# Performance work log

Measured on AMD Instinct MI355X. Metric: run time of the kernel, lower is better.

Reference implementation:

```python
import jax, jax.numpy as jnp
import numpy as np

IN_SIZE = 256
HIDDEN = 512
T = 32768


def setup_inputs() -> dict:
    key = jax.random.key(0)
    ks = jax.random.split(key, 6)
    lim_ih = 1.0 / np.sqrt(HIDDEN)
    inp = {
        "input": jax.random.normal(ks[0], (T, IN_SIZE), dtype=jnp.float32),
        "init_hidden": jax.random.normal(ks[1], (HIDDEN,), dtype=jnp.float32),
        # eqx.nn.GRUCell parameters: weight_ih (3H, in), weight_hh (3H, H), bias (3H,), bias_n (H,)
        "weight_ih": jax.random.uniform(ks[2], (3 * HIDDEN, IN_SIZE), minval=-lim_ih, maxval=lim_ih, dtype=jnp.float32),
        "weight_hh": jax.random.uniform(ks[3], (3 * HIDDEN, HIDDEN), minval=-lim_ih, maxval=lim_ih, dtype=jnp.float32),
        "bias": jax.random.uniform(ks[4], (3 * HIDDEN,), minval=-lim_ih, maxval=lim_ih, dtype=jnp.float32),
        "bias_n": jax.random.uniform(ks[5], (HIDDEN,), minval=-lim_ih, maxval=lim_ih, dtype=jnp.float32),
    }
    return inp


def reference(input, init_hidden, weight_ih, weight_hh, bias, bias_n):
    H = init_hidden.shape[0]
    # Precompute all input-side gates in one big GEMM: [T, 3H]
    igates_all = input @ weight_ih.T + bias

    def step(h, ig):
        hg = weight_hh @ h  # [3H]
        ir, iz, inn = ig[:H], ig[H:2 * H], ig[2 * H:]
        hr, hz, hn = hg[:H], hg[H:2 * H], hg[2 * H:]
        reset = jax.nn.sigmoid(ir + hr)
        upd = jax.nn.sigmoid(iz + hz)
        new = jnp.tanh(inn + reset * (hn + bias_n))
        h_new = new + upd * (h - new)
        # rnn_out_o = atleast_2d(h_new) -> (1, H); [..., 0] -> (1,)
        return h_new, h_new[:1]

    _, out = jax.lax.scan(step, init_hidden, igates_all)
    return out  # [T, 1]
```

## Files before the change

### kernel.cpp

```cpp
#include <hip/hip_runtime.h>


#define T_STEPS    32768
#define INSZ       256
#define HSZ        512
#define TPB        768
#define NWG        32
#define POLL_GUARD 16384

typedef unsigned long long u64;
typedef unsigned int u32;
typedef u32 u32x4 __attribute__((ext_vector_type(4)));
typedef float f32x4 __attribute__((ext_vector_type(4)));
typedef float f32x2 __attribute__((ext_vector_type(2)));

__device__ __forceinline__ float grp_reduce16(float v) {
  v += __shfl_xor(v, 1);
  v += __shfl_xor(v, 2);
  v += __shfl_xor(v, 4);
  v += __shfl_xor(v, 8);
  return v;
}

__device__ __forceinline__ int hpad(int k) { return k + 4 * (k >> 5); }

__device__ __forceinline__ void st16_sys(u64* p, u32x4 v) {
  asm volatile("global_store_dwordx4 %0, %1, off sc0 sc1" :: "v"(p), "v"(v) : "memory");
}

__global__ void init_comm(u64* __restrict__ comm, const float* __restrict__ h0) {
  int jj = threadIdx.x;
  u32 bits = __float_as_uint(h0[jj]);
  comm[jj]       = (u64)bits;
  comm[HSZ + jj] = 0xFFFFFFFF00000000ull;
}

__launch_bounds__(TPB, 1)
__global__ void gru_persistent(const float* __restrict__ input,
                               const float* __restrict__ init_hidden,
                               const float* __restrict__ w_ih,
                               const float* __restrict__ w_hh,
                               const float* __restrict__ bias,
                               const float* __restrict__ bias_n,
                               u64* __restrict__ comm,
                               float* __restrict__ out)
{
  const int tid = threadIdx.x;
  const int wg  = blockIdx.x;
  const int g   = tid >> 4;
  const int l   = tid & 15;
  const int R   = wg * 16 + (g & 15) + 512 * (g >> 4);

  f32x4 whh[8];
  f32x4 wih[4];
  {
    const float* rp = w_hh + (size_t)R * HSZ + l * 32;
    #pragma unroll
    for (int c = 0; c < 8; ++c) whh[c] = *(const f32x4*)(rp + c * 4);
    const float* rp2 = w_ih + (size_t)R * INSZ + l * 16;
    #pragma unroll
    for (int c = 0; c < 4; ++c) wih[c] = *(const f32x4*)(rp2 + c * 4);
  }

  float hold = 0.f, b_r = 0.f, b_z = 0.f, b_n = 0.f, bn = 0.f;
  if (tid < 16) {
    const int j = wg * 16 + tid;
    hold = init_hidden[j];
    b_r  = bias[j];
    b_z  = bias[j + 512];
    b_n  = bias[j + 1024];
    bn   = bias_n[j];
  }

  __shared__ float h_lds[2][HSZ + 4 * (HSZ >> 5)];
  __shared__ float gsum[48];
  __shared__ float isum[2][48];
  __shared__ float xstage[INSZ];

  if (tid < 64) {
    f32x4 v = *(const f32x4*)(input + tid * 4);
    *(f32x4*)&xstage[tid * 4] = v;
  }
  __syncthreads();
  {
    float a = 0.f;
    #pragma unroll
    for (int c = 0; c < 4; ++c) {
      f32x4 xv = *(const f32x4*)&xstage[l * 16 + c * 4];
      #pragma unroll
      for (int u = 0; u < 4; ++u) a += wih[c][u] * xv[u];
    }
    a = grp_reduce16(a);
    if (l == 0) isum[0][g] = a;
  }

  const int poller = (tid >= 256 && tid < 512);
  const int pt     = tid - 256;
  const int stager = (tid >= 512 && tid < 576);
  u32x4 pa, pb, pc, pd, win;

#define ISSUE(Rr) \
  asm volatile("global_load_dwordx4 %0, %1, off sc0 sc1" : "=&v"(Rr) : "v"(lp) : "memory")
#define CHECK(Rr) \
  asm volatile("s_waitcnt vmcnt(3)" : "+v"(Rr)); \
  __builtin_amdgcn_sched_barrier(0); \
  if ((Rr[1] == tt && Rr[3] == tt) || --guard == 0) { win = Rr; break; } \
  ISSUE(Rr)

  for (int t = 0; t < T_STEPS; ++t) {
    const int p  = t & 1;
    const u32 tt = (u32)t;

    if (poller) {
      const u64* lp = comm + (size_t)p * HSZ + 2 * pt;
      ISSUE(pa); ISSUE(pb); ISSUE(pc); ISSUE(pd);
      int guard = POLL_GUARD;
      for (;;) {
        CHECK(pa);
        CHECK(pb);
        CHECK(pc);
        CHECK(pd);
      }
      f32x2 hv;
      hv[0] = __uint_as_float(win[0]);
      hv[1] = __uint_as_float(win[2]);
      *(f32x2*)&h_lds[p][hpad(2 * pt)] = hv;
    }
    f32x4 xnew = {0.f, 0.f, 0.f, 0.f};
    if (stager) {
      const int tn = (t + 1 < T_STEPS) ? (t + 1) : (T_STEPS - 1);
      xnew = *(const f32x4*)(input + (size_t)tn * INSZ + (tid - 512) * 4);
    }
    __syncthreads();

    float a = 0.f;
    {
      const float* hp = &h_lds[p][l * 36];
      #pragma unroll
      for (int c = 0; c < 8; ++c) {
        f32x4 hv4 = *(const f32x4*)(hp + c * 4);
        #pragma unroll
        for (int u = 0; u < 4; ++u) a += whh[c][u] * hv4[u];
      }
    }
    a = grp_reduce16(a);
    if (l == 0) gsum[g] = a;
    if (stager) *(f32x4*)&xstage[(tid - 512) * 4] = xnew;
    __syncthreads();

    if (tid < 16) {
      const int j = tid;
      const float hr = gsum[j], hz = gsum[16 + j], hn = gsum[32 + j];
      const float i_r = isum[p][j], i_z = isum[p][16 + j], i_n = isum[p][32 + j];
      const float reset = 1.0f / (1.0f + __expf(-(i_r + b_r + hr)));
      const float upd   = 1.0f / (1.0f + __expf(-(i_z + b_z + hz)));
      const float newv  = tanhf(i_n + b_n + reset * (hn + bn));
      const float hnew  = newv + upd * (hold - newv);
      hold = hnew;
      const float hpair = __shfl(hnew, tid + 1);
      if ((j & 1) == 0) {
        u64* nbuf = comm + (size_t)((t + 1) & 1) * HSZ;
        u32x4 pk;
        pk[0] = __float_as_uint(hnew);  pk[1] = (u32)(t + 1);
        pk[2] = __float_as_uint(hpair); pk[3] = (u32)(t + 1);
        st16_sys(&nbuf[wg * 16 + j], pk);
        if (wg == 0 && j == 0) out[t] = hnew;
      }
    }

    {
      float a2 = 0.f;
      #pragma unroll
      for (int c = 0; c < 4; ++c) {
        f32x4 xv = *(const f32x4*)&xstage[l * 16 + c * 4];
        #pragma unroll
        for (int u = 0; u < 4; ++u) a2 += wih[c][u] * xv[u];
      }
      a2 = grp_reduce16(a2);
      if (l == 0) isum[(t + 1) & 1][g] = a2;
    }
  }
#undef ISSUE
#undef CHECK
}

extern "C" void kernel_launch(void* const* d_in, const int* in_sizes, int n_in,
                              void* d_out, int out_size, void* d_ws, size_t ws_size,
                              hipStream_t stream) {
  const float* input  = (const float*)d_in[0];
  const float* h0     = (const float*)d_in[1];
  const float* w_ih   = (const float*)d_in[2];
  const float* w_hh   = (const float*)d_in[3];
  const float* bias   = (const float*)d_in[4];
  const float* bias_n = (const float*)d_in[5];
  float* out = (float*)d_out;
  u64* comm  = (u64*)d_ws;

  hipLaunchKernelGGL(init_comm, dim3(1), dim3(HSZ), 0, stream, comm, h0);
  hipLaunchKernelGGL(gru_persistent, dim3(NWG), dim3(TPB), 0, stream,
                     input, h0, w_ih, w_hh, bias, bias_n, comm, out);
}
```

Before: 57.91 ms.

## Separate poller waves from matvec waves, pad x staging, use fast gate math

Raises the block to 1024 threads so the 256 polling threads (waves 12-15) no longer overlap the threads that hold weights and compute the matvec. The staging of the next input row moves to threads 64-127 and is issued before polling so the load overlaps the wait. The x staging buffer is padded to avoid LDS bank conflicts. Sigmoid and tanh now use hardware reciprocal and exp instead of division and tanhf, which shortens the serial gate update at a small accuracy cost. The extra waves add scheduling overhead and may raise barrier cost.

```diff
diff --git a/kernel.cpp b/kernel.cpp
--- a/kernel.cpp
+++ b/kernel.cpp
@@ -4,7 +4,7 @@
 #define T_STEPS    32768
 #define INSZ       256
 #define HSZ        512
-#define TPB        768
+#define TPB        1024
 #define NWG        32
 #define POLL_GUARD 16384
 
@@ -23,6 +23,7 @@
 }
 
 __device__ __forceinline__ int hpad(int k) { return k + 4 * (k >> 5); }
+__device__ __forceinline__ int xpad(int k) { return k + ((k >> 4) << 2); }
 
 __device__ __forceinline__ void st16_sys(u64* p, u32x4 v) {
   asm volatile("global_store_dwordx4 %0, %1, off sc0 sc1" :: "v"(p), "v"(v) : "memory");
@@ -49,11 +50,12 @@
   const int wg  = blockIdx.x;
   const int g   = tid >> 4;
   const int l   = tid & 15;
+  const bool mv = (g < 48);
   const int R   = wg * 16 + (g & 15) + 512 * (g >> 4);
 
   f32x4 whh[8];
   f32x4 wih[4];
-  {
+  if (mv) {
     const float* rp = w_hh + (size_t)R * HSZ + l * 32;
     #pragma unroll
     for (int c = 0; c < 8; ++c) whh[c] = *(const f32x4*)(rp + c * 4);
@@ -75,18 +77,19 @@
   __shared__ float h_lds[2][HSZ + 4 * (HSZ >> 5)];
   __shared__ float gsum[48];
   __shared__ float isum[2][48];
-  __shared__ float xstage[INSZ];
-
-  if (tid < 64) {
-    f32x4 v = *(const f32x4*)(input + tid * 4);
-    *(f32x4*)&xstage[tid * 4] = v;
+  __shared__ float xstage[INSZ + (INSZ >> 4) * 4];
+
+  if (tid >= 64 && tid < 128) {
+    const int s = tid - 64;
+    f32x4 v = *(const f32x4*)(input + s * 4);
+    *(f32x4*)&xstage[xpad(s * 4)] = v;
   }
   __syncthreads();
-  {
+  if (mv) {
     float a = 0.f;
     #pragma unroll
     for (int c = 0; c < 4; ++c) {
-      f32x4 xv = *(const f32x4*)&xstage[l * 16 + c * 4];
+      f32x4 xv = *(const f32x4*)&xstage[20 * l + 4 * c];
       #pragma unroll
       for (int u = 0; u < 4; ++u) a += wih[c][u] * xv[u];
     }
@@ -94,9 +97,8 @@
     if (l == 0) isum[0][g] = a;
   }
 
-  const int poller = (tid >= 256 && tid < 512);
-  const int pt     = tid - 256;
-  const int stager = (tid >= 512 && tid < 576);
+  const bool poller = (tid >= 768);
+  const int  pt     = tid - 768;
   u32x4 pa, pb, pc, pd, win;
 
 #define ISSUE(Rr) \
@@ -110,6 +112,12 @@
   for (int t = 0; t < T_STEPS; ++t) {
     const int p  = t & 1;
     const u32 tt = (u32)t;
+
+    f32x4 xnew = {0.f, 0.f, 0.f, 0.f};
+    if (tid >= 64 && tid < 128) {
+      const int tn = (t + 1 < T_STEPS) ? (t + 1) : (T_STEPS - 1);
+      xnew = *(const f32x4*)(input + (size_t)tn * INSZ + (tid - 64) * 4);
+    }
 
     if (poller) {
       const u64* lp = comm + (size_t)p * HSZ + 2 * pt;
@@ -126,15 +134,10 @@
       hv[1] = __uint_as_float(win[2]);
       *(f32x2*)&h_lds[p][hpad(2 * pt)] = hv;
     }
-    f32x4 xnew = {0.f, 0.f, 0.f, 0.f};
-    if (stager) {
-      const int tn = (t + 1 < T_STEPS) ? (t + 1) : (T_STEPS - 1);
-      xnew = *(const f32x4*)(input + (size_t)tn * INSZ + (tid - 512) * 4);
-    }
     __syncthreads();
 
-    float a = 0.f;
-    {
+    if (mv) {
+      float a = 0.f;
       const float* hp = &h_lds[p][l * 36];
       #pragma unroll
       for (int c = 0; c < 8; ++c) {
@@ -142,19 +145,20 @@
         #pragma unroll
         for (int u = 0; u < 4; ++u) a += whh[c][u] * hv4[u];
       }
-    }
-    a = grp_reduce16(a);
-    if (l == 0) gsum[g] = a;
-    if (stager) *(f32x4*)&xstage[(tid - 512) * 4] = xnew;
+      a = grp_reduce16(a);
+      if (l == 0) gsum[g] = a;
+    }
+    if (tid >= 64 && tid < 128) *(f32x4*)&xstage[xpad((tid - 64) * 4)] = xnew;
     __syncthreads();
 
     if (tid < 16) {
       const int j = tid;
       const float hr = gsum[j], hz = gsum[16 + j], hn = gsum[32 + j];
       const float i_r = isum[p][j], i_z = isum[p][16 + j], i_n = isum[p][32 + j];
-      const float reset = 1.0f / (1.0f + __expf(-(i_r + b_r + hr)));
-      const float upd   = 1.0f / (1.0f + __expf(-(i_z + b_z + hz)));
-      const float newv  = tanhf(i_n + b_n + reset * (hn + bn));
+      const float reset = __builtin_amdgcn_rcpf(1.0f + __expf(-(i_r + b_r + hr)));
+      const float upd   = __builtin_amdgcn_rcpf(1.0f + __expf(-(i_z + b_z + hz)));
+      const float e2    = __expf(2.0f * (i_n + b_n + reset * (hn + bn)));
+      const float newv  = 1.0f - 2.0f * __builtin_amdgcn_rcpf(1.0f + e2);
       const float hnew  = newv + upd * (hold - newv);
       hold = hnew;
       const float hpair = __shfl(hnew, tid + 1);
@@ -168,11 +172,11 @@
       }
     }
 
-    {
+    if (mv) {
       float a2 = 0.f;
       #pragma unroll
       for (int c = 0; c < 4; ++c) {
-        f32x4 xv = *(const f32x4*)&xstage[l * 16 + c * 4];
+        f32x4 xv = *(const f32x4*)&xstage[20 * l + 4 * c];
         #pragma unroll
         for (int u = 0; u < 4; ++u) a2 += wih[c][u] * xv[u];
       }
```

New measurement: 51.76 ms. 1.12x faster.
